# Optimization experiments

Hardware: AMD Instinct MI355X
Metric: run time of the kernel (lower is better)

The kernel has to match this reference:

```python
import jax, jax.numpy as jnp
import numpy as np

NUM_HEADS = 8  # from init_kwargs


def setup_inputs() -> dict:
    key = jax.random.key(0)
    ks = jax.random.split(key, 8)
    B, N, Din, H, Dout, E = 4, 2048, 256, 512, 256, 65536
    s = 0.02
    return {
        "x": jax.random.normal(ks[0], (B, N, Din), jnp.float32),
        "edge_index": jax.random.randint(ks[1], (2, E), 0, N),
        "W_gcn": jax.random.normal(ks[2], (Din, H), jnp.float32) * s,
        "b_gcn": jnp.zeros((H,), jnp.float32),
        "in_proj_w": jax.random.normal(ks[3], (3 * H, H), jnp.float32) * s,
        "in_proj_b": jnp.zeros((3 * H,), jnp.float32),
        "out_proj_w": jax.random.normal(ks[4], (H, H), jnp.float32) * s,
        "out_proj_b": jnp.zeros((H,), jnp.float32),
        "fc_w": jax.random.normal(ks[5], (H, Dout), jnp.float32) * s,
        "fc_b": jnp.zeros((Dout,), jnp.float32),
    }


def _gcn(x, edge_index, W, b):
    # PyG GCNConv: add self-loops, symmetric normalization, gather-scatter aggregation.
    B, N, _ = x.shape
    loop = jnp.arange(N)
    src = jnp.concatenate([edge_index[0], loop])  # message source j
    dst = jnp.concatenate([edge_index[1], loop])  # aggregation target i
    deg = jnp.zeros((N,), x.dtype).at[dst].add(1.0)
    dinv = jnp.where(deg > 0, jax.lax.rsqrt(deg), 0.0)
    norm = dinv[src] * dinv[dst]                  # [Etot]
    xl = x @ W                                    # [B, N, H]
    msgs = xl[:, src, :] * norm[None, :, None]    # [B, Etot, H]
    out = jnp.zeros_like(xl).at[:, dst].add(msgs)  # scatter-add over edges
    return out + b


def _mha(x_nbh, wi, bi, wo, bo, nh):
    # torch MultiheadAttention, input [N(seq), B, H], self-attention.
    N, B, H = x_nbh.shape
    dh = H // nh
    qkv = x_nbh @ wi.T + bi                       # [N, B, 3H]
    q, k, v = jnp.split(qkv, 3, axis=-1)
    q = q.reshape(N, B, nh, dh) * (dh ** -0.5)
    k = k.reshape(N, B, nh, dh)
    v = v.reshape(N, B, nh, dh)
    scores = jnp.einsum("nbhd,mbhd->bhnm", q, k)  # [B, nh, N, N]
    attn = jax.nn.softmax(scores, axis=-1)
    o = jnp.einsum("bhnm,mbhd->nbhd", attn, v).reshape(N, B, H)
    return o @ wo.T + bo


def reference(x, edge_index, W_gcn, b_gcn, in_proj_w, in_proj_b,
              out_proj_w, out_proj_b, fc_w, fc_b):
    h = _gcn(x, edge_index, W_gcn, b_gcn)         # [B, N, H]
    h = jnp.transpose(h, (1, 0, 2))               # [N, B, H]
    h = _mha(h, in_proj_w, in_proj_b, out_proj_w, out_proj_b, NUM_HEADS)
    h = jnp.transpose(h, (1, 0, 2))               # [B, N, H]
    h = jax.nn.relu(h)
    return h @ fc_w + fc_b                        # [B, N, Dout]
```

## Files before the change

### kernel.cpp

```cpp
#include <hip/hip_runtime.h>
#include <hip/hip_bf16.h>


#define NN 2048
#define HH 512
#define NHEAD 8
#define DH 64

typedef _Float16 f16;
typedef __attribute__((ext_vector_type(2))) _Float16 f16x2;
typedef __attribute__((ext_vector_type(4))) _Float16 f16x4;
typedef __attribute__((ext_vector_type(8))) _Float16 f16x8;
typedef __attribute__((ext_vector_type(4))) float f32x4;

#define GLOAD_LDS16(g, l)                                              \
  __builtin_amdgcn_global_load_lds(                                    \
      (const __attribute__((address_space(1))) void*)(g),              \
      (__attribute__((address_space(3))) void*)(l), 16, 0, 0)


__global__ __launch_bounds__(256) void prep_cvt_kernel(const float* __restrict__ wi,
                                                       const float* __restrict__ wo,
                                                       f16* __restrict__ wi16,
                                                       f16* __restrict__ wo16,
                                                       float* __restrict__ deg,
                                                       int* __restrict__ cursor) {
  const int bid = blockIdx.x, t = threadIdx.x;
  if (bid < 768) {
    const int i = bid * 256 + t;
    const float4 v = ((const float4*)wi)[i];
    f16x4 o = { (f16)v.x, (f16)v.y, (f16)v.z, (f16)v.w };
    ((f16x4*)wi16)[i] = o;
  } else if (bid < 1024) {
    const int i = (bid - 768) * 256 + t;
    const float4 v = ((const float4*)wo)[i];
    f16x4 o = { (f16)v.x, (f16)v.y, (f16)v.z, (f16)v.w };
    ((f16x4*)wo16)[i] = o;
  } else {
    for (int i = t; i < NN; i += 256) { deg[i] = 1.0f; cursor[i] = 0; }
  }
}

__global__ __launch_bounds__(256) void prep_transpose_kernel(const float* __restrict__ wg,
                                                             const float* __restrict__ fcw,
                                                             f16* __restrict__ wg16t,
                                                             f16* __restrict__ fcw16t) {
  __shared__ float tbuf[32][33];
  const float* in;
  f16* outp;
  int R, C, bx, by;
  if (blockIdx.x < 128) { in = wg;  outp = wg16t;  R = 256; C = 512;
                          bx = blockIdx.x & 15; by = blockIdx.x >> 4; }
  else { int id = blockIdx.x - 128; in = fcw; outp = fcw16t; R = 512; C = 256;
         bx = id & 7; by = id >> 3; }
  const int c0 = bx * 32, r0 = by * 32;
  const int tx = threadIdx.x & 31, ty = threadIdx.x >> 5;
#pragma unroll
  for (int i = 0; i < 32; i += 8) tbuf[ty + i][tx] = in[(size_t)(r0 + ty + i) * C + c0 + tx];
  __syncthreads();
#pragma unroll
  for (int i = 0; i < 32; i += 8)
    outp[(size_t)(c0 + ty + i) * R + r0 + tx] = (f16)tbuf[tx][ty + i];
}


__global__ __launch_bounds__(256) void count_deg_kernel(const int* __restrict__ ei, int E,
                                                        float* __restrict__ deg) {
  int e = blockIdx.x * 256 + threadIdx.x;
  if (e < E) atomicAdd(&deg[ei[E + e]], 1.0f);
}

__global__ __launch_bounds__(1024) void build_rowptr_kernel(const float* __restrict__ deg,
                                                            float* __restrict__ dinv,
                                                            int* __restrict__ rowptr) {
  __shared__ int a[NN];
  __shared__ int bbuf[NN];
  const int t = threadIdx.x;
  for (int i = t; i < NN; i += 1024) {
    float dg = deg[i];
    a[i] = (int)dg - 1;
    dinv[i] = rsqrtf(dg);
  }
  __syncthreads();
  int* src = a;
  int* dst = bbuf;
  for (int off = 1; off < NN; off <<= 1) {
    for (int i = t; i < NN; i += 1024) {
      int v = src[i];
      if (i >= off) v += src[i - off];
      dst[i] = v;
    }
    __syncthreads();
    int* tmp = src; src = dst; dst = tmp;
  }
  for (int i = t; i < NN; i += 1024) rowptr[i + 1] = src[i];
  if (t == 0) rowptr[0] = 0;
}

__global__ __launch_bounds__(256) void fill_csr_kernel(const int* __restrict__ ei, int E,
                                                       const int* __restrict__ rowptr,
                                                       int* __restrict__ cursor,
                                                       int* __restrict__ csr_src) {
  int e = blockIdx.x * 256 + threadIdx.x;
  if (e < E) {
    int s = ei[e];
    int d = ei[E + e];
    int pos = atomicAdd(&cursor[d], 1);
    csr_src[rowptr[d] + pos] = s;
  }
}


template <int OUTMODE, bool BIAS, bool RELU, bool AF32, int MT = 128>
__global__ __launch_bounds__(256) void mfma_gemm_kernel(
    const void* __restrict__ Ap, const f16* __restrict__ Bt,
    const float* __restrict__ bias, void* __restrict__ Cout,
    int M, int N, int K,
    f16* __restrict__ q_out, f16* __restrict__ k_out, f16* __restrict__ v_out) {
  constexpr int MI = MT / 32;
  __shared__ f16 As[MT * 32];
  __shared__ f16 Bs[128 * 32];
  const int tid = threadIdx.x;
  const int wave = tid >> 6, lane = tid & 63;
  const int quad = lane >> 4, l16 = lane & 15;
  const int m0 = blockIdx.y * MT, n0 = blockIdx.x * 128;
  const int moff = (wave >> 1) * (MI * 16), noff = (wave & 1) * 64;

  f32x4 acc[MI][4];
#pragma unroll
  for (int i = 0; i < MI; ++i)
#pragma unroll
    for (int j = 0; j < 4; ++j) acc[i][j] = (f32x4){0.f, 0.f, 0.f, 0.f};

  const int rpw = MT / 4;
  const int srowA = rpw * wave + (lane >> 2);
  const int srowB = 32 * wave + (lane >> 2);
  const int kch = (lane & 3) * 8;
  const f16* Ag = (const f16*)Ap + (size_t)(m0 + srowA) * K + kch;
  const float* Ag32 = (const float*)Ap + (size_t)(m0 + srowA) * K + kch;
  const f16* Bg = Bt + (size_t)(n0 + srowB) * K + kch;
  f16* As_w = &As[(rpw * wave) * 32];
  f16* Bs_w = &Bs[(32 * wave) * 32];

  for (int k0 = 0; k0 < K; k0 += 32) {
    __syncthreads();
    if (AF32) {
#pragma unroll
      for (int t = 0; t < 2; ++t) {
        const float* g = Ag32 + k0 + (size_t)(16 * t) * K;
        const float4 u0 = *(const float4*)g;
        const float4 u1 = *(const float4*)(g + 4);
        f16x8 o = { (f16)u0.x, (f16)u0.y, (f16)u0.z, (f16)u0.w,
                    (f16)u1.x, (f16)u1.y, (f16)u1.z, (f16)u1.w };
        *(f16x8*)&As[(srowA + 16 * t) * 32 + kch] = o;
      }
    } else {
      GLOAD_LDS16(Ag + k0, As_w);
      if (MT == 128) GLOAD_LDS16(Ag + k0 + (size_t)16 * K, As_w + 16 * 32);
    }
    GLOAD_LDS16(Bg + k0, Bs_w);
    GLOAD_LDS16(Bg + k0 + (size_t)16 * K, Bs_w + 16 * 32);
    __syncthreads();
    f16x8 af[MI], bf[4];
#pragma unroll
    for (int m16 = 0; m16 < MI; ++m16)
      af[m16] = *(const f16x8*)&As[(moff + m16 * 16 + l16) * 32 + quad * 8];
#pragma unroll
    for (int n16 = 0; n16 < 4; ++n16)
      bf[n16] = *(const f16x8*)&Bs[(noff + n16 * 16 + l16) * 32 + quad * 8];
#pragma unroll
    for (int m16 = 0; m16 < MI; ++m16)
#pragma unroll
      for (int n16 = 0; n16 < 4; ++n16)
        acc[m16][n16] =
            __builtin_amdgcn_mfma_f32_16x16x32_f16(af[m16], bf[n16], acc[m16][n16], 0, 0, 0);
  }

  float bv[4];
#pragma unroll
  for (int n16 = 0; n16 < 4; ++n16)
    bv[n16] = BIAS ? bias[n0 + noff + n16 * 16 + l16] : 0.f;

  if (OUTMODE == 2) {
    const int hblk = (n0 >> 6) + (wave & 1);
    const int which = hblk >> 3, h = hblk & 7;
    f16* dst = (which == 0) ? q_out : (which == 1) ? k_out : v_out;
    const float scale = (which == 0) ? 0.125f : 1.0f;
#pragma unroll
    for (int m16 = 0; m16 < MI; ++m16) {
#pragma unroll
      for (int r = 0; r < 4; ++r) {
        const int m = m0 + moff + m16 * 16 + quad * 4 + r;
        const int b = m >> 11, ns = m & 2047;
        f16* row = dst + ((size_t)(b * 8 + h) * NN + ns) * DH;
#pragma unroll
        for (int n16 = 0; n16 < 4; ++n16) {
          const int d = n16 * 16 + l16;
          row[d] = (f16)((acc[m16][n16][r] + bv[n16]) * scale);
        }
      }
    }
  } else {
#pragma unroll
    for (int m16 = 0; m16 < MI; ++m16) {
#pragma unroll
      for (int r = 0; r < 4; ++r) {
        const size_t row = (size_t)(m0 + moff + m16 * 16 + quad * 4 + r) * N;
#pragma unroll
        for (int n16 = 0; n16 < 4; ++n16) {
          const int col = n0 + noff + n16 * 16 + l16;
          float v = acc[m16][n16][r] + bv[n16];
          if (RELU) v = fmaxf(v, 0.f);
          if (OUTMODE == 0) ((float*)Cout)[row + col] = v;
          else ((f16*)Cout)[row + col] = (f16)v;
        }
      }
    }
  }
}


__global__ __launch_bounds__(256) void gcn_aggregate_kernel(const f16* __restrict__ xl,
                                                            const float* __restrict__ dinv,
                                                            const int* __restrict__ rowptr,
                                                            const int* __restrict__ csr_src,
                                                            const float* __restrict__ b_gcn,
                                                            f16* __restrict__ out) {
  __shared__ int s_src[256];
  __shared__ float s_dv[256];
  const int i = blockIdx.x;
  const int tid = threadIdx.x;
  const float dv_i = dinv[i];
  const int f = tid * 2;
  float ax[4], ay[4];
#pragma unroll
  for (int b = 0; b < 4; ++b) {
    const f16x2 self = *(const f16x2*)&xl[((size_t)(b * NN) + i) * HH + f];
    ax[b] = (float)self.x * dv_i;
    ay[b] = (float)self.y * dv_i;
  }
  const int beg = rowptr[i], end = rowptr[i + 1];
  for (int c0 = beg; c0 < end; c0 += 256) {
    const int cnt = min(256, end - c0);
    __syncthreads();
    if (tid < cnt) {
      int s = csr_src[c0 + tid];
      s_src[tid] = s;
      s_dv[tid] = dinv[s];
    }
    __syncthreads();
    for (int t = 0; t < cnt; ++t) {
      const int row = s_src[t];
      const float w = s_dv[t];
#pragma unroll
      for (int b = 0; b < 4; ++b) {
        const f16x2 v = *(const f16x2*)&xl[((size_t)(b * NN) + row) * HH + f];
        ax[b] = fmaf((float)v.x, w, ax[b]);
        ay[b] = fmaf((float)v.y, w, ay[b]);
      }
    }
  }
  const float2 bg = *(const float2*)&b_gcn[f];
#pragma unroll
  for (int b = 0; b < 4; ++b) {
    f16x2 o = { (f16)(ax[b] * dv_i + bg.x), (f16)(ay[b] * dv_i + bg.y) };
    *(f16x2*)&out[((size_t)(b * NN) + i) * HH + f] = o;
  }
}


__global__ __launch_bounds__(256) void flash_attn_f16_kernel(const f16* __restrict__ Qb,
                                                             const f16* __restrict__ Kb,
                                                             const f16* __restrict__ Vb,
                                                             f16* __restrict__ out) {
  const int LDK = 72;
  const int LDV = 136;
  __shared__ f16 Ks[128 * LDK];
  __shared__ f16 Vt[64 * LDV];
  const int tid = threadIdx.x;
  const int wave = tid >> 6, lane = tid & 63;
  const int quad = lane >> 4, l16 = lane & 15;
  const int n0 = blockIdx.x * 128;
  const int bh = blockIdx.y;
  const int b = bh >> 3, h = bh & 7;
  const f16* kb = Kb + (size_t)bh * NN * DH;
  const f16* vb = Vb + (size_t)bh * NN * DH;

  f16x8 aq[2][2];
#pragma unroll
  for (int g = 0; g < 2; ++g) {
    const f16* qf = Qb + ((size_t)bh * NN + n0 + (wave + 4 * g) * 16 + l16) * DH + quad * 8;
    aq[g][0] = *(const f16x8*)qf;
    aq[g][1] = *(const f16x8*)(qf + 32);
  }

  float l_part[2] = {0.f, 0.f};
  f32x4 acc_o[2][4];
#pragma unroll
  for (int g = 0; g < 2; ++g)
#pragma unroll
    for (int n16 = 0; n16 < 4; ++n16) acc_o[g][n16] = (f32x4){0.f, 0.f, 0.f, 0.f};

  const int vdg = tid & 15, jbb = tid >> 4;

  for (int kt = 0; kt < NN / 128; ++kt) {
    const int k0 = kt * 128;
    __syncthreads();
#pragma unroll
    for (int i = 0; i < 4; ++i) {
      int idx = tid + 256 * i;
      int r = idx >> 3, koff = (idx & 7) * 8;
      *(f16x8*)&Ks[r * LDK + koff] = *(const f16x8*)(kb + (size_t)(k0 + r) * DH + koff);
    }
#pragma unroll
    for (int cc = 0; cc < 2; ++cc) {
      const int jb = jbb + 16 * cc;
      const int sb4 = (jb >> 3) * 32 + (jb & 3) * 8 + ((jb >> 2) & 1) * 4;
      f16x4 vv[4];
#pragma unroll
      for (int i = 0; i < 4; ++i)
        vv[i] = *(const f16x4*)(vb + (size_t)(k0 + jb * 4 + i) * DH + vdg * 4);
#pragma unroll
      for (int c = 0; c < 4; ++c) {
        f16x4 o = { vv[0][c], vv[1][c], vv[2][c], vv[3][c] };
        *(f16x4*)&Vt[(vdg * 4 + c) * LDV + sb4] = o;
      }
    }
    __syncthreads();
#pragma unroll
    for (int p = 0; p < 4; ++p) {
      f32x4 sA[2][2];
#pragma unroll
      for (int t = 0; t < 2; ++t) {
        const f16x8 ak0 = *(const f16x8*)&Ks[(p * 32 + t * 16 + l16) * LDK + quad * 8];
        const f16x8 ak1 = *(const f16x8*)&Ks[(p * 32 + t * 16 + l16) * LDK + quad * 8 + 32];
#pragma unroll
        for (int g = 0; g < 2; ++g) {
          f32x4 s = {0.f, 0.f, 0.f, 0.f};
          s = __builtin_amdgcn_mfma_f32_16x16x32_f16(ak0, aq[g][0], s, 0, 0, 0);
          s = __builtin_amdgcn_mfma_f32_16x16x32_f16(ak1, aq[g][1], s, 0, 0, 0);
          sA[g][t] = s;
        }
      }
      f16x8 bvv[4];
#pragma unroll
      for (int n16 = 0; n16 < 4; ++n16)
        bvv[n16] = *(const f16x8*)&Vt[(n16 * 16 + l16) * LDV + p * 32 + quad * 8];
#pragma unroll
      for (int g = 0; g < 2; ++g) {
        f16x8 ap;
        float sum = 0.f;
#pragma unroll
        for (int t = 0; t < 2; ++t)
#pragma unroll
          for (int r = 0; r < 4; ++r) {
            const float e = __expf(sA[g][t][r]);
            sum += e;
            ap[t * 4 + r] = (f16)e;
          }
        l_part[g] += sum;
#pragma unroll
        for (int n16 = 0; n16 < 4; ++n16)
          acc_o[g][n16] = __builtin_amdgcn_mfma_f32_16x16x32_f16(ap, bvv[n16], acc_o[g][n16], 0, 0, 0);
      }
    }
  }
#pragma unroll
  for (int g = 0; g < 2; ++g) {
    float lp = l_part[g];
    lp += __shfl_xor(lp, 16);
    lp += __shfl_xor(lp, 32);
    f16* obase = out + ((size_t)b * NN + n0 + (wave + 4 * g) * 16) * HH + h * DH;
#pragma unroll
    for (int r = 0; r < 4; ++r) {
      const float lr = __shfl(lp, (lane & 48) | (quad * 4 + r));
      const float inv = 1.0f / lr;
#pragma unroll
      for (int n16 = 0; n16 < 4; ++n16)
        obase[(size_t)(quad * 4 + r) * HH + n16 * 16 + l16] = (f16)(acc_o[g][n16][r] * inv);
    }
  }
}


extern "C" void kernel_launch(void* const* d_in, const int* in_sizes, int n_in,
                              void* d_out, int out_size, void* d_ws, size_t ws_size,
                              hipStream_t stream) {
  const float* x     = (const float*)d_in[0];
  const int*   ei    = (const int*)d_in[1];
  const float* W_gcn = (const float*)d_in[2];
  const float* b_gcn = (const float*)d_in[3];
  const float* wi    = (const float*)d_in[4];
  const float* bi    = (const float*)d_in[5];
  const float* wo    = (const float*)d_in[6];
  const float* bo    = (const float*)d_in[7];
  const float* fcw   = (const float*)d_in[8];
  const float* fcb   = (const float*)d_in[9];
  float* out = (float*)d_out;
  const int E = in_sizes[1] / 2;
  const int M = 4 * NN;

  char* wsb = (char*)d_ws;
  const size_t MB = 1u << 20;
  f16* xl16   = (f16*)(wsb + 4 * MB);
  f16* hb16   = (f16*)(wsb + 12 * MB);
  f16* Qb     = (f16*)(wsb + 20 * MB);
  f16* Kb     = (f16*)(wsb + 28 * MB);
  f16* Vb     = (f16*)(wsb + 36 * MB);
  f16* attn16 = (f16*)(wsb + 44 * MB);
  f16* proj16 = (f16*)(wsb + 52 * MB);
  f16* wi16   = (f16*)(wsb + 60 * MB);
  f16* wo16   = (f16*)(wsb + 62 * MB);
  f16* wg16t  = (f16*)(wsb + 63 * MB);
  f16* fcw16t = (f16*)(wsb + 64 * MB);
  float* deg  = (float*)(wsb + 65 * MB);
  float* dinv = deg + NN;
  int* rowptr = (int*)(dinv + NN);
  int* cursor = rowptr + 2080;
  int* csr    = cursor + NN;

  prep_cvt_kernel<<<1025, 256, 0, stream>>>(wi, wo, wi16, wo16, deg, cursor);
  prep_transpose_kernel<<<256, 256, 0, stream>>>(W_gcn, fcw, wg16t, fcw16t);

  count_deg_kernel<<<(E + 255) / 256, 256, 0, stream>>>(ei, E, deg);
  build_rowptr_kernel<<<1, 1024, 0, stream>>>(deg, dinv, rowptr);
  fill_csr_kernel<<<(E + 255) / 256, 256, 0, stream>>>(ei, E, rowptr, cursor, csr);

  mfma_gemm_kernel<1, false, false, true><<<dim3(4, 64), 256, 0, stream>>>(
      x, wg16t, nullptr, xl16, M, 512, 256, nullptr, nullptr, nullptr);
  gcn_aggregate_kernel<<<NN, 256, 0, stream>>>(xl16, dinv, rowptr, csr, b_gcn, hb16);
  mfma_gemm_kernel<2, true, false, false><<<dim3(12, 64), 256, 0, stream>>>(
      hb16, wi16, bi, nullptr, M, 1536, 512, Qb, Kb, Vb);
  flash_attn_f16_kernel<<<dim3(NN / 128, 32), 256, 0, stream>>>(Qb, Kb, Vb, attn16);
  mfma_gemm_kernel<1, true, true, false><<<dim3(4, 64), 256, 0, stream>>>(
      attn16, wo16, bo, proj16, M, 512, 512, nullptr, nullptr, nullptr);
  mfma_gemm_kernel<0, true, false, false, 64><<<dim3(2, 128), 256, 0, stream>>>(
      proj16, fcw16t, fcb, out, M, 256, 512, nullptr, nullptr, nullptr);
}
```

Baseline: 261.2 us.

## Split attention over two key halves and vectorize GCN aggregation loads

The flash-attention kernel now splits the key range into two halves across a third grid dimension. Each half writes unnormalized partial outputs and row sums, and a new combine kernel adds the halves and normalizes them. This doubles the block count from 512 so more of the GPU's compute units stay busy. The GCN aggregation kernel now gives each wave one batch and 8 features per thread, using 16-byte loads instead of 4-byte ones. The cost is an extra kernel launch and an extra round trip of partial outputs through memory. Skipping the max subtraction appears to rely on the score range staying bounded, as it already did before.

```diff
diff --git a/kernel.cpp b/kernel.cpp
--- a/kernel.cpp
+++ b/kernel.cpp
@@ -230,14 +230,15 @@
   __shared__ float s_dv[256];
   const int i = blockIdx.x;
   const int tid = threadIdx.x;
+  const int b = tid >> 6;
+  const int f = (tid & 63) * 8;
   const float dv_i = dinv[i];
-  const int f = tid * 2;
-  float ax[4], ay[4];
-#pragma unroll
-  for (int b = 0; b < 4; ++b) {
-    const f16x2 self = *(const f16x2*)&xl[((size_t)(b * NN) + i) * HH + f];
-    ax[b] = (float)self.x * dv_i;
-    ay[b] = (float)self.y * dv_i;
+  const f16* xb = xl + (size_t)b * NN * HH;
+  float acc[8];
+  {
+    const f16x8 self = *(const f16x8*)&xb[(size_t)i * HH + f];
+#pragma unroll
+    for (int c = 0; c < 8; ++c) acc[c] = (float)self[c] * dv_i;
   }
   const int beg = rowptr[i], end = rowptr[i + 1];
   for (int c0 = beg; c0 < end; c0 += 256) {
@@ -250,29 +251,32 @@
     }
     __syncthreads();
     for (int t = 0; t < cnt; ++t) {
-      const int row = s_src[t];
+      const f16x8 v = *(const f16x8*)&xb[(size_t)s_src[t] * HH + f];
       const float w = s_dv[t];
 #pragma unroll
-      for (int b = 0; b < 4; ++b) {
-        const f16x2 v = *(const f16x2*)&xl[((size_t)(b * NN) + row) * HH + f];
-        ax[b] = fmaf((float)v.x, w, ax[b]);
-        ay[b] = fmaf((float)v.y, w, ay[b]);
-      }
-    }
-  }
-  const float2 bg = *(const float2*)&b_gcn[f];
-#pragma unroll
-  for (int b = 0; b < 4; ++b) {
-    f16x2 o = { (f16)(ax[b] * dv_i + bg.x), (f16)(ay[b] * dv_i + bg.y) };
-    *(f16x2*)&out[((size_t)(b * NN) + i) * HH + f] = o;
-  }
+      for (int c = 0; c < 8; ++c) acc[c] = fmaf((float)v[c], w, acc[c]);
+    }
+  }
+  const float4 bg0 = *(const float4*)&b_gcn[f];
+  const float4 bg1 = *(const float4*)&b_gcn[f + 4];
+  f16x8 o;
+  o[0] = (f16)(acc[0] * dv_i + bg0.x);
+  o[1] = (f16)(acc[1] * dv_i + bg0.y);
+  o[2] = (f16)(acc[2] * dv_i + bg0.z);
+  o[3] = (f16)(acc[3] * dv_i + bg0.w);
+  o[4] = (f16)(acc[4] * dv_i + bg1.x);
+  o[5] = (f16)(acc[5] * dv_i + bg1.y);
+  o[6] = (f16)(acc[6] * dv_i + bg1.z);
+  o[7] = (f16)(acc[7] * dv_i + bg1.w);
+  *(f16x8*)&out[((size_t)b * NN + i) * HH + f] = o;
 }
 
 
 __global__ __launch_bounds__(256) void flash_attn_f16_kernel(const f16* __restrict__ Qb,
                                                              const f16* __restrict__ Kb,
                                                              const f16* __restrict__ Vb,
-                                                             f16* __restrict__ out) {
+                                                             f16* __restrict__ Op,
+                                                             float* __restrict__ Lp) {
   const int LDK = 72;
   const int LDV = 136;
   __shared__ f16 Ks[128 * LDK];
@@ -282,6 +286,7 @@
   const int quad = lane >> 4, l16 = lane & 15;
   const int n0 = blockIdx.x * 128;
   const int bh = blockIdx.y;
+  const int kh = blockIdx.z;
   const int b = bh >> 3, h = bh & 7;
   const f16* kb = Kb + (size_t)bh * NN * DH;
   const f16* vb = Vb + (size_t)bh * NN * DH;
@@ -303,7 +308,7 @@
 
   const int vdg = tid & 15, jbb = tid >> 4;
 
-  for (int kt = 0; kt < NN / 128; ++kt) {
+  for (int kt = kh * 8; kt < kh * 8 + 8; ++kt) {
     const int k0 = kt * 128;
     __syncthreads();
 #pragma unroll
@@ -365,21 +370,39 @@
       }
     }
   }
+  f16* ohalf = Op + (size_t)kh * 4 * NN * HH;
 #pragma unroll
   for (int g = 0; g < 2; ++g) {
     float lp = l_part[g];
     lp += __shfl_xor(lp, 16);
     lp += __shfl_xor(lp, 32);
-    f16* obase = out + ((size_t)b * NN + n0 + (wave + 4 * g) * 16) * HH + h * DH;
-#pragma unroll
-    for (int r = 0; r < 4; ++r) {
-      const float lr = __shfl(lp, (lane & 48) | (quad * 4 + r));
-      const float inv = 1.0f / lr;
+    const int qrow = n0 + (wave + 4 * g) * 16;
+    if (quad == 0) Lp[(size_t)(kh * 32 + bh) * NN + qrow + l16] = lp;
+    f16* obase = ohalf + ((size_t)b * NN + qrow) * HH + h * DH;
+#pragma unroll
+    for (int r = 0; r < 4; ++r)
 #pragma unroll
       for (int n16 = 0; n16 < 4; ++n16)
-        obase[(size_t)(quad * 4 + r) * HH + n16 * 16 + l16] = (f16)(acc_o[g][n16][r] * inv);
-    }
-  }
+        obase[(size_t)(quad * 4 + r) * HH + n16 * 16 + l16] = (f16)acc_o[g][n16][r];
+  }
+}
+
+__global__ __launch_bounds__(256) void attn_combine_kernel(const f16* __restrict__ Op,
+                                                           const float* __restrict__ Lp,
+                                                           f16* __restrict__ attn) {
+  const int idx = blockIdx.x * 256 + threadIdx.x;
+  const int row = idx >> 7, c4 = (idx & 127) * 4;
+  const int h = c4 >> 6;
+  const int b = row >> 11, n = row & 2047;
+  const int bh = b * 8 + h;
+  const float l = Lp[(size_t)bh * NN + n] + Lp[(size_t)(32 + bh) * NN + n];
+  const float inv = 1.0f / l;
+  const f16x4 a0 = *(const f16x4*)&Op[(size_t)row * HH + c4];
+  const f16x4 a1 = *(const f16x4*)&Op[(size_t)(4 * NN + row) * HH + c4];
+  f16x4 o;
+#pragma unroll
+  for (int c = 0; c < 4; ++c) o[c] = (f16)(((float)a0[c] + (float)a1[c]) * inv);
+  *(f16x4*)&attn[(size_t)row * HH + c4] = o;
 }
 
 
@@ -404,6 +427,7 @@
   const size_t MB = 1u << 20;
   f16* xl16   = (f16*)(wsb + 4 * MB);
   f16* hb16   = (f16*)(wsb + 12 * MB);
+  f16* Opart  = (f16*)(wsb + 4 * MB);
   f16* Qb     = (f16*)(wsb + 20 * MB);
   f16* Kb     = (f16*)(wsb + 28 * MB);
   f16* Vb     = (f16*)(wsb + 36 * MB);
@@ -418,6 +442,7 @@
   int* rowptr = (int*)(dinv + NN);
   int* cursor = rowptr + 2080;
   int* csr    = cursor + NN;
+  float* Lpart = (float*)(wsb + 66 * MB);
 
   prep_cvt_kernel<<<1025, 256, 0, stream>>>(wi, wo, wi16, wo16, deg, cursor);
   prep_transpose_kernel<<<256, 256, 0, stream>>>(W_gcn, fcw, wg16t, fcw16t);
@@ -431,7 +456,8 @@
   gcn_aggregate_kernel<<<NN, 256, 0, stream>>>(xl16, dinv, rowptr, csr, b_gcn, hb16);
   mfma_gemm_kernel<2, true, false, false><<<dim3(12, 64), 256, 0, stream>>>(
       hb16, wi16, bi, nullptr, M, 1536, 512, Qb, Kb, Vb);
-  flash_attn_f16_kernel<<<dim3(NN / 128, 32), 256, 0, stream>>>(Qb, Kb, Vb, attn16);
+  flash_attn_f16_kernel<<<dim3(NN / 128, 32, 2), 256, 0, stream>>>(Qb, Kb, Vb, Opart, Lpart);
+  attn_combine_kernel<<<M * (HH / 4) / 256, 256, 0, stream>>>(Opart, Lpart, attn16);
   mfma_gemm_kernel<1, true, true, false><<<dim3(4, 64), 256, 0, stream>>>(
       attn16, wo16, bo, proj16, M, 512, 512, nullptr, nullptr, nullptr);
   mfma_gemm_kernel<0, true, false, false, 64><<<dim3(2, 128), 256, 0, stream>>>(
```

After: 263.9 us. No clear change (+1.0%).
